# Kernel optimization log

Measured on AMD Instinct MI355X. Metric: run time of the kernel, lower is better.

The kernel has to match this reference:

```python
import jax, jax.numpy as jnp
import numpy as np
from jax import lax

D_MODEL = 1024
KERNEL = 7
EPS = 1e-8


def setup_inputs() -> dict:
    key = jax.random.key(0)
    ks = jax.random.split(key, 8)
    B, T, D = 4, 4096, D_MODEL
    x = jax.random.normal(ks[0], (B, T, D), dtype=jnp.float32)
    # rotary tables [T, D/2]
    pos = jnp.arange(T, dtype=jnp.float32)[:, None]
    inv_freq = 1.0 / (10000.0 ** (jnp.arange(D // 2, dtype=jnp.float32) / (D // 2)))
    ang = pos * inv_freq[None, :]
    sin = jnp.sin(ang)
    cos = jnp.cos(ang)
    # params
    W_proj = jax.random.normal(ks[1], (D, 2 * D), dtype=jnp.float32) * (1.0 / np.sqrt(D))
    b_proj = jnp.zeros((2 * D,), dtype=jnp.float32)
    dw_kernel = jax.random.normal(ks[2], (KERNEL, 1, D), dtype=jnp.float32) * 0.1  # [K,1,C] WIO depthwise
    dw_bias = jnp.zeros((D,), dtype=jnp.float32)
    gamma = jnp.ones((D,), dtype=jnp.float32)
    return {"x": x, "sin": sin, "cos": cos, "W_proj": W_proj, "b_proj": b_proj,
            "dw_kernel": dw_kernel, "dw_bias": dw_bias, "gamma": gamma}


def reference(x, sin, cos, W_proj, b_proj, dw_kernel, dw_bias, gamma):
    D = D_MODEL
    proj = jnp.einsum('btd,df->btf', x, W_proj) + b_proj          # [B,T,2D]
    x_a, x_b = proj[..., :D], proj[..., D:]
    # interleaved rotary: even/odd pairs
    x1 = x_a[..., 0::2]                                            # [B,T,D/2]
    x2 = x_a[..., 1::2]
    c = cos[None, :, :]
    s = sin[None, :, :]
    r1 = x1 * c - x2 * s
    r2 = x1 * s + x2 * c
    x_rot = jnp.stack([r1, r2], axis=-1).reshape(x_a.shape)        # re-interleave
    # depthwise conv1d, SAME padding
    conv = lax.conv_general_dilated(
        x_rot, dw_kernel, window_strides=(1,), padding='SAME',
        dimension_numbers=('NWC', 'WIO', 'NWC'), feature_group_count=D) + dw_bias
    act = conv * jax.nn.sigmoid(conv)                              # swish
    gated = act * jax.nn.sigmoid(x_b)
    rms = jnp.sqrt(jnp.mean(jnp.square(gated), axis=-1, keepdims=True) + EPS)
    return gamma * (gated / rms)
```

## Files before the change

### kernel.cpp

```cpp
#include <hip/hip_runtime.h>
#include <stdint.h>

#define D_MODEL 1024
#define T_LEN   4096
#define B_SZ    4
#define NROWS   (B_SZ * T_LEN)
#define NPROJ   (2 * D_MODEL)
#define CHUNK   16

#define BM 256
#define BN 256
#define BK 64
#define NT (D_MODEL / BK)

typedef __attribute__((ext_vector_type(8))) __bf16 bf16x8;
typedef __attribute__((ext_vector_type(4))) float  f32x4;

using as1_void = __attribute__((address_space(1))) void;
using as3_void = __attribute__((address_space(3))) void;

__device__ inline float bf2f(unsigned short u) {
    union { unsigned int i; float f; } v; v.i = ((unsigned int)u) << 16; return v.f;
}
__device__ inline unsigned short f2bf(float f) {
    union { float f; unsigned int i; } v; v.f = f;
    return (unsigned short)((v.i + 0x7fffu + ((v.i >> 16) & 1u)) >> 16);
}
__device__ inline float sigmoidf(float x) { return 1.0f / (1.0f + __expf(-x)); }

__global__ __launch_bounds__(256) void k_cvt_x(const float* __restrict__ x,
                                               unsigned short* __restrict__ xb) {
    int i = (blockIdx.x * 256 + threadIdx.x) * 4;
    float4 v = *reinterpret_cast<const float4*>(x + i);
    ushort4 o;
    o.x = f2bf(v.x); o.y = f2bf(v.y); o.z = f2bf(v.z); o.w = f2bf(v.w);
    *reinterpret_cast<ushort4*>(xb + i) = o;
}

__global__ __launch_bounds__(256) void k_cvt_w(const float* __restrict__ W,
                                               unsigned short* __restrict__ wt) {
    __shared__ unsigned short tile[32][33];
    int n0 = blockIdx.x * 32, k0 = blockIdx.y * 32;
    int c = threadIdx.x & 31, r = threadIdx.x >> 5;
    #pragma unroll
    for (int i = 0; i < 4; i++) {
        int kk = r + i * 8;
        tile[kk][c] = f2bf(W[(uint64_t)(k0 + kk) * NPROJ + n0 + c]);
    }
    __syncthreads();
    #pragma unroll
    for (int i = 0; i < 4; i++) {
        int nn = r + i * 8;
        wt[(uint64_t)(n0 + nn) * D_MODEL + k0 + c] = tile[c][nn];
    }
}

__global__ __launch_bounds__(512, 2) void k_gemm(const unsigned short* __restrict__ xb,
                                                 const unsigned short* __restrict__ wt,
                                                 const float* __restrict__ bias,
                                                 unsigned short* __restrict__ projb) {
    __shared__ __align__(16) unsigned short As[2 * BM * BK];
    __shared__ __align__(16) unsigned short Bs[2 * BM * BK];

    const int tid  = threadIdx.x;
    const int lane = tid & 63;
    const int w    = tid >> 6;
    const int wm   = w >> 2;
    const int wn   = w & 3;

    const int bid = blockIdx.x;
    const int wg  = (bid & 7) * 64 + (bid >> 3);
    const int n0  = (wg >> 6) * BN;
    const int m0  = (wg & 63) * BM;

    const int srow = tid >> 3;
    const int scol = ((tid & 7) ^ (srow & 7)) * 8;
    const int fr   = lane & 15;
    const int fq   = lane >> 4;

    f32x4 acc[8][4] = {};

    auto STAGE = [&](int buf, int ks) {
        #pragma unroll
        for (int i = 0; i < 4; ++i) {
            const unsigned short* ga = xb + (uint64_t)(m0 + i * 64 + srow) * D_MODEL + ks + scol;
            __builtin_amdgcn_global_load_lds((as1_void*)(void*)ga,
                (as3_void*)(void*)&As[buf * (BM * BK) + i * 4096 + w * 512], 16, 0, 0);
        }
        #pragma unroll
        for (int i = 0; i < 4; ++i) {
            const unsigned short* gb = wt + (uint64_t)(n0 + i * 64 + srow) * D_MODEL + ks + scol;
            __builtin_amdgcn_global_load_lds((as1_void*)(void*)gb,
                (as3_void*)(void*)&Bs[buf * (BM * BK) + i * 4096 + w * 512], 16, 0, 0);
        }
    };

    STAGE(0, 0);
    __syncthreads();

    for (int t = 0; t < NT; ++t) {
        const int cur = t & 1;
        if (t + 1 < NT) STAGE(1 - cur, (t + 1) * BK);

        const unsigned short* Ab = &As[cur * (BM * BK)];
        const unsigned short* Bb = &Bs[cur * (BM * BK)];
        #pragma unroll
        for (int kk = 0; kk < BK; kk += 32) {
            const int slot = (kk >> 3) + fq;
            bf16x8 b[4];
            #pragma unroll
            for (int n = 0; n < 4; n++) {
                const int rb = wn * 64 + n * 16 + fr;
                b[n] = *reinterpret_cast<const bf16x8*>(&Bb[rb * 64 + ((slot ^ (fr & 7)) * 8)]);
            }
            #pragma unroll
            for (int m = 0; m < 8; m++) {
                const int ra = wm * 128 + m * 16 + fr;
                bf16x8 a = *reinterpret_cast<const bf16x8*>(&Ab[ra * 64 + ((slot ^ (fr & 7)) * 8)]);
                #pragma unroll
                for (int n = 0; n < 4; n++)
                    acc[m][n] = __builtin_amdgcn_mfma_f32_16x16x32_bf16(a, b[n], acc[m][n], 0, 0, 0);
            }
        }
        __syncthreads();
    }

    #pragma unroll
    for (int m = 0; m < 8; m++) {
        const int grow = m0 + wm * 128 + m * 16 + fq * 4;
        #pragma unroll
        for (int n = 0; n < 4; n++) {
            const int gcol = n0 + wn * 64 + n * 16 + fr;
            const float bv = bias[gcol];
            #pragma unroll
            for (int r = 0; r < 4; r++) {
                projb[(uint64_t)(grow + r) * NPROJ + gcol] = f2bf(acc[m][n][r] + bv);
            }
        }
    }
}

__global__ __launch_bounds__(512) void k_post(const unsigned short* __restrict__ projb,
                                              const float* __restrict__ sinp,
                                              const float* __restrict__ cosp,
                                              const float* __restrict__ kw,
                                              const float* __restrict__ dwb,
                                              const float* __restrict__ gamma,
                                              float* __restrict__ out) {
    const int blk  = blockIdx.x;
    const int b    = blk / (T_LEN / CHUNK);
    const int t0   = (blk % (T_LEN / CHUNK)) * CHUNK;
    const int c    = threadIdx.x;
    const int d0   = c * 2;
    const uint64_t bbase = (uint64_t)b * T_LEN;

    float kwv[7][2];
    #pragma unroll
    for (int j = 0; j < 7; j++) {
        kwv[j][0] = kw[j * D_MODEL + d0];
        kwv[j][1] = kw[j * D_MODEL + d0 + 1];
    }
    const float bv0 = dwb[d0], bv1 = dwb[d0 + 1];
    const float gm0 = gamma[d0], gm1 = gamma[d0 + 1];

    __shared__ float red[2][8];

    auto load_rope = [&](int tj, float& o0, float& o1) {
        if ((unsigned)tj < (unsigned)T_LEN) {
            ushort2 u = *reinterpret_cast<const ushort2*>(projb + (bbase + tj) * NPROJ + d0);
            float cv = cosp[(uint64_t)tj * (D_MODEL / 2) + c];
            float sv = sinp[(uint64_t)tj * (D_MODEL / 2) + c];
            float x0 = bf2f(u.x), x1 = bf2f(u.y);
            o0 = x0 * cv - x1 * sv;
            o1 = x0 * sv + x1 * cv;
        } else { o0 = 0.f; o1 = 0.f; }
    };

    float rg[6][2];
    #pragma unroll
    for (int j = 0; j < 6; j++) load_rope(t0 - 3 + j, rg[j][0], rg[j][1]);
    float nx0, nx1;
    load_rope(t0 + 3, nx0, nx1);

    ushort2 xb_cur = *reinterpret_cast<const ushort2*>(projb + (bbase + t0) * NPROJ + D_MODEL + d0);

    for (int t = t0; t < t0 + CHUNK; ++t) {
        const float r60 = nx0, r61 = nx1;

        float acc0 = rg[0][0] * kwv[0][0] + rg[1][0] * kwv[1][0] + rg[2][0] * kwv[2][0]
                   + rg[3][0] * kwv[3][0] + rg[4][0] * kwv[4][0] + rg[5][0] * kwv[5][0]
                   + r60 * kwv[6][0] + bv0;
        float acc1 = rg[0][1] * kwv[0][1] + rg[1][1] * kwv[1][1] + rg[2][1] * kwv[2][1]
                   + rg[3][1] * kwv[3][1] + rg[4][1] * kwv[4][1] + rg[5][1] * kwv[5][1]
                   + r61 * kwv[6][1] + bv1;

        load_rope(t + 4, nx0, nx1);
        const ushort2 xb_use = xb_cur;
        if (t + 1 < t0 + CHUNK) {
            xb_cur = *reinterpret_cast<const ushort2*>(projb + (bbase + t + 1) * NPROJ + D_MODEL + d0);
        }

        float a0 = acc0 * sigmoidf(acc0);
        float a1 = acc1 * sigmoidf(acc1);
        float g0 = a0 * sigmoidf(bf2f(xb_use.x));
        float g1 = a1 * sigmoidf(bf2f(xb_use.y));

        float ssq = g0 * g0 + g1 * g1;
        #pragma unroll
        for (int off = 32; off; off >>= 1) ssq += __shfl_down(ssq, off);
        const int p = t & 1;
        if ((threadIdx.x & 63) == 0) red[p][threadIdx.x >> 6] = ssq;
        __syncthreads();
        float total = red[p][0] + red[p][1] + red[p][2] + red[p][3]
                    + red[p][4] + red[p][5] + red[p][6] + red[p][7];
        const float inv = 1.0f / sqrtf(total * (1.0f / (float)D_MODEL) + 1e-8f);

        float2 o;
        o.x = g0 * inv * gm0;
        o.y = g1 * inv * gm1;
        *reinterpret_cast<float2*>(out + (bbase + t) * D_MODEL + d0) = o;

        #pragma unroll
        for (int j = 0; j < 5; j++) { rg[j][0] = rg[j + 1][0]; rg[j][1] = rg[j + 1][1]; }
        rg[5][0] = r60; rg[5][1] = r61;
    }
}

extern "C" void kernel_launch(void* const* d_in, const int* in_sizes, int n_in,
                              void* d_out, int out_size, void* d_ws, size_t ws_size,
                              hipStream_t stream) {
    const float* x     = (const float*)d_in[0];
    const float* sinp  = (const float*)d_in[1];
    const float* cosp  = (const float*)d_in[2];
    const float* W     = (const float*)d_in[3];
    const float* bproj = (const float*)d_in[4];
    const float* dwk   = (const float*)d_in[5];
    const float* dwb   = (const float*)d_in[6];
    const float* gamma = (const float*)d_in[7];
    float* out = (float*)d_out;

    unsigned short* xb    = (unsigned short*)d_ws;
    unsigned short* wt    = xb + (size_t)NROWS * D_MODEL;
    unsigned short* projb = wt + (size_t)NPROJ * D_MODEL;

    k_cvt_x<<<(NROWS * D_MODEL) / (256 * 4), 256, 0, stream>>>(x, xb);
    k_cvt_w<<<dim3(NPROJ / 32, D_MODEL / 32), 256, 0, stream>>>(W, wt);
    k_gemm<<<(NPROJ / BN) * (NROWS / BM), 512, 0, stream>>>(xb, wt, bproj, projb);
    k_post<<<B_SZ * (T_LEN / CHUNK), 512, 0, stream>>>(projb, sinp, cosp, dwk, dwb, gamma, out);
}
```

Baseline: 149.0 us.

## Deepen GEMM pipeline to 4-stage LDS ring with BK=32 and manual vmcnt waits

```diff
diff --git a/kernel.cpp b/kernel.cpp
--- a/kernel.cpp
+++ b/kernel.cpp
@@ -10,8 +10,9 @@
 
 #define BM 256
 #define BN 256
-#define BK 64
-#define NT (D_MODEL / BK)
+#define BK2 32
+#define NT2 (D_MODEL / BK2)
+#define NBUF 4
 
 typedef __attribute__((ext_vector_type(8))) __bf16 bf16x8;
 typedef __attribute__((ext_vector_type(4))) float  f32x4;
@@ -59,8 +60,8 @@
                                                  const unsigned short* __restrict__ wt,
                                                  const float* __restrict__ bias,
                                                  unsigned short* __restrict__ projb) {
-    __shared__ __align__(16) unsigned short As[2 * BM * BK];
-    __shared__ __align__(16) unsigned short Bs[2 * BM * BK];
+    __shared__ __align__(16) unsigned short As[NBUF * BM * BK2];
+    __shared__ __align__(16) unsigned short Bs[NBUF * BM * BK2];
 
     const int tid  = threadIdx.x;
     const int lane = tid & 63;
@@ -73,56 +74,65 @@
     const int n0  = (wg >> 6) * BN;
     const int m0  = (wg & 63) * BM;
 
-    const int srow = tid >> 3;
-    const int scol = ((tid & 7) ^ (srow & 7)) * 8;
+    const int srow = tid >> 2;
+    const int skey = (tid >> 3) & 3;
+    const int scol = ((tid & 3) ^ skey) * 8;
     const int fr   = lane & 15;
     const int fq   = lane >> 4;
 
     f32x4 acc[8][4] = {};
 
-    auto STAGE = [&](int buf, int ks) {
-        #pragma unroll
-        for (int i = 0; i < 4; ++i) {
-            const unsigned short* ga = xb + (uint64_t)(m0 + i * 64 + srow) * D_MODEL + ks + scol;
+    auto STAGE = [&](int tk) {
+        const int buf = tk & 3;
+        const int ks  = tk * BK2;
+        #pragma unroll
+        for (int i = 0; i < 2; ++i) {
+            const unsigned short* ga = xb + (uint64_t)(m0 + i * 128 + srow) * D_MODEL + ks + scol;
             __builtin_amdgcn_global_load_lds((as1_void*)(void*)ga,
-                (as3_void*)(void*)&As[buf * (BM * BK) + i * 4096 + w * 512], 16, 0, 0);
-        }
-        #pragma unroll
-        for (int i = 0; i < 4; ++i) {
-            const unsigned short* gb = wt + (uint64_t)(n0 + i * 64 + srow) * D_MODEL + ks + scol;
+                (as3_void*)(void*)&As[buf * 8192 + i * 4096 + w * 512], 16, 0, 0);
+        }
+        #pragma unroll
+        for (int i = 0; i < 2; ++i) {
+            const unsigned short* gb = wt + (uint64_t)(n0 + i * 128 + srow) * D_MODEL + ks + scol;
             __builtin_amdgcn_global_load_lds((as1_void*)(void*)gb,
-                (as3_void*)(void*)&Bs[buf * (BM * BK) + i * 4096 + w * 512], 16, 0, 0);
+                (as3_void*)(void*)&Bs[buf * 8192 + i * 4096 + w * 512], 16, 0, 0);
         }
     };
 
-    STAGE(0, 0);
-    __syncthreads();
-
-    for (int t = 0; t < NT; ++t) {
-        const int cur = t & 1;
-        if (t + 1 < NT) STAGE(1 - cur, (t + 1) * BK);
-
-        const unsigned short* Ab = &As[cur * (BM * BK)];
-        const unsigned short* Bb = &Bs[cur * (BM * BK)];
-        #pragma unroll
-        for (int kk = 0; kk < BK; kk += 32) {
-            const int slot = (kk >> 3) + fq;
-            bf16x8 b[4];
+    STAGE(0); STAGE(1); STAGE(2);
+    asm volatile("s_waitcnt vmcnt(8)" ::: "memory");
+    __builtin_amdgcn_s_barrier();
+    __builtin_amdgcn_sched_barrier(0);
+
+    for (int t = 0; t < NT2; ++t) {
+        if (t + 3 < NT2) STAGE(t + 3);
+
+        const unsigned short* Ab = &As[(t & 3) * 8192];
+        const unsigned short* Bb = &Bs[(t & 3) * 8192];
+        bf16x8 a[8], b[4];
+        #pragma unroll
+        for (int n = 0; n < 4; n++) {
+            const int rb = wn * 64 + n * 16 + fr;
+            b[n] = *reinterpret_cast<const bf16x8*>(&Bb[rb * 32 + ((fq ^ ((rb >> 1) & 3)) * 8)]);
+        }
+        #pragma unroll
+        for (int m = 0; m < 8; m++) {
+            const int ra = wm * 128 + m * 16 + fr;
+            a[m] = *reinterpret_cast<const bf16x8*>(&Ab[ra * 32 + ((fq ^ ((ra >> 1) & 3)) * 8)]);
+        }
+        #pragma unroll
+        for (int m = 0; m < 8; m++)
             #pragma unroll
-            for (int n = 0; n < 4; n++) {
-                const int rb = wn * 64 + n * 16 + fr;
-                b[n] = *reinterpret_cast<const bf16x8*>(&Bb[rb * 64 + ((slot ^ (fr & 7)) * 8)]);
-            }
-            #pragma unroll
-            for (int m = 0; m < 8; m++) {
-                const int ra = wm * 128 + m * 16 + fr;
-                bf16x8 a = *reinterpret_cast<const bf16x8*>(&Ab[ra * 64 + ((slot ^ (fr & 7)) * 8)]);
-                #pragma unroll
-                for (int n = 0; n < 4; n++)
-                    acc[m][n] = __builtin_amdgcn_mfma_f32_16x16x32_bf16(a, b[n], acc[m][n], 0, 0, 0);
-            }
-        }
-        __syncthreads();
+            for (int n = 0; n < 4; n++)
+                acc[m][n] = __builtin_amdgcn_mfma_f32_16x16x32_bf16(a[m], b[n], acc[m][n], 0, 0, 0);
+
+        if (t < NT2 - 1) {
+            if (t + 3 < NT2)      asm volatile("s_waitcnt vmcnt(8)" ::: "memory");
+            else if (t + 2 < NT2) asm volatile("s_waitcnt vmcnt(4)" ::: "memory");
+            else                  asm volatile("s_waitcnt vmcnt(0)" ::: "memory");
+            __builtin_amdgcn_s_barrier();
+            __builtin_amdgcn_sched_barrier(0);
+        }
     }
 
     #pragma unroll
```

Result: slower. 162.2 us (+8.9%).

## Fuse rotary and gate sigmoid into GEMM epilogue, merge convert kernels

Applied to the files above, without the earlier changes.

```diff
diff --git a/kernel.cpp b/kernel.cpp
--- a/kernel.cpp
+++ b/kernel.cpp
@@ -28,36 +28,41 @@
 }
 __device__ inline float sigmoidf(float x) { return 1.0f / (1.0f + __expf(-x)); }
 
-__global__ __launch_bounds__(256) void k_cvt_x(const float* __restrict__ x,
-                                               unsigned short* __restrict__ xb) {
-    int i = (blockIdx.x * 256 + threadIdx.x) * 4;
-    float4 v = *reinterpret_cast<const float4*>(x + i);
-    ushort4 o;
-    o.x = f2bf(v.x); o.y = f2bf(v.y); o.z = f2bf(v.z); o.w = f2bf(v.w);
-    *reinterpret_cast<ushort4*>(xb + i) = o;
-}
-
-__global__ __launch_bounds__(256) void k_cvt_w(const float* __restrict__ W,
-                                               unsigned short* __restrict__ wt) {
+__global__ __launch_bounds__(256) void k_cvt(const float* __restrict__ x,
+                                             unsigned short* __restrict__ xb,
+                                             const float* __restrict__ W,
+                                             unsigned short* __restrict__ wt) {
     __shared__ unsigned short tile[32][33];
-    int n0 = blockIdx.x * 32, k0 = blockIdx.y * 32;
-    int c = threadIdx.x & 31, r = threadIdx.x >> 5;
-    #pragma unroll
-    for (int i = 0; i < 4; i++) {
-        int kk = r + i * 8;
-        tile[kk][c] = f2bf(W[(uint64_t)(k0 + kk) * NPROJ + n0 + c]);
-    }
-    __syncthreads();
-    #pragma unroll
-    for (int i = 0; i < 4; i++) {
-        int nn = r + i * 8;
-        wt[(uint64_t)(n0 + nn) * D_MODEL + k0 + c] = tile[c][nn];
+    int bid = blockIdx.x;
+    if (bid < (NROWS * D_MODEL) / (256 * 4)) {
+        int i = (bid * 256 + threadIdx.x) * 4;
+        float4 v = *reinterpret_cast<const float4*>(x + i);
+        ushort4 o;
+        o.x = f2bf(v.x); o.y = f2bf(v.y); o.z = f2bf(v.z); o.w = f2bf(v.w);
+        *reinterpret_cast<ushort4*>(xb + i) = o;
+    } else {
+        bid -= (NROWS * D_MODEL) / (256 * 4);
+        int n0 = (bid & 63) * 32, k0 = (bid >> 6) * 32;
+        int c = threadIdx.x & 31, r = threadIdx.x >> 5;
+        #pragma unroll
+        for (int i = 0; i < 4; i++) {
+            int kk = r + i * 8;
+            tile[kk][c] = f2bf(W[(uint64_t)(k0 + kk) * NPROJ + n0 + c]);
+        }
+        __syncthreads();
+        #pragma unroll
+        for (int i = 0; i < 4; i++) {
+            int nn = r + i * 8;
+            wt[(uint64_t)(n0 + nn) * D_MODEL + k0 + c] = tile[c][nn];
+        }
     }
 }
 
 __global__ __launch_bounds__(512, 2) void k_gemm(const unsigned short* __restrict__ xb,
                                                  const unsigned short* __restrict__ wt,
                                                  const float* __restrict__ bias,
+                                                 const float* __restrict__ sinp,
+                                                 const float* __restrict__ cosp,
                                                  unsigned short* __restrict__ projb) {
     __shared__ __align__(16) unsigned short As[2 * BM * BK];
     __shared__ __align__(16) unsigned short Bs[2 * BM * BK];
@@ -125,24 +130,46 @@
         __syncthreads();
     }
 
-    #pragma unroll
-    for (int m = 0; m < 8; m++) {
-        const int grow = m0 + wm * 128 + m * 16 + fq * 4;
-        #pragma unroll
-        for (int n = 0; n < 4; n++) {
-            const int gcol = n0 + wn * 64 + n * 16 + fr;
-            const float bv = bias[gcol];
-            #pragma unroll
-            for (int r = 0; r < 4; r++) {
-                projb[(uint64_t)(grow + r) * NPROJ + gcol] = f2bf(acc[m][n][r] + bv);
+    if (n0 < D_MODEL) {
+        #pragma unroll
+        for (int m = 0; m < 8; m++) {
+            const int grow = m0 + wm * 128 + m * 16 + fq * 4;
+            #pragma unroll
+            for (int n = 0; n < 4; n++) {
+                const int gcol = n0 + wn * 64 + n * 16 + fr;
+                const float bv = bias[gcol];
+                const int pidx = gcol >> 1;
+                const bool evn = (gcol & 1) == 0;
+                #pragma unroll
+                for (int r = 0; r < 4; r++) {
+                    const int trow = (grow + r) & (T_LEN - 1);
+                    float v = acc[m][n][r] + bv;
+                    float other = __shfl_xor(v, 1);
+                    float cv = cosp[(uint64_t)trow * (D_MODEL / 2) + pidx];
+                    float sv = sinp[(uint64_t)trow * (D_MODEL / 2) + pidx];
+                    float ro = evn ? (v * cv - other * sv) : (other * sv + v * cv);
+                    projb[(uint64_t)(grow + r) * NPROJ + gcol] = f2bf(ro);
+                }
+            }
+        }
+    } else {
+        #pragma unroll
+        for (int m = 0; m < 8; m++) {
+            const int grow = m0 + wm * 128 + m * 16 + fq * 4;
+            #pragma unroll
+            for (int n = 0; n < 4; n++) {
+                const int gcol = n0 + wn * 64 + n * 16 + fr;
+                const float bv = bias[gcol];
+                #pragma unroll
+                for (int r = 0; r < 4; r++) {
+                    projb[(uint64_t)(grow + r) * NPROJ + gcol] = f2bf(sigmoidf(acc[m][n][r] + bv));
+                }
             }
         }
     }
 }
 
 __global__ __launch_bounds__(512) void k_post(const unsigned short* __restrict__ projb,
-                                              const float* __restrict__ sinp,
-                                              const float* __restrict__ cosp,
                                               const float* __restrict__ kw,
                                               const float* __restrict__ dwb,
                                               const float* __restrict__ gamma,
@@ -165,22 +192,18 @@
 
     __shared__ float red[2][8];
 
-    auto load_rope = [&](int tj, float& o0, float& o1) {
+    auto load_row = [&](int tj, float& o0, float& o1) {
         if ((unsigned)tj < (unsigned)T_LEN) {
             ushort2 u = *reinterpret_cast<const ushort2*>(projb + (bbase + tj) * NPROJ + d0);
-            float cv = cosp[(uint64_t)tj * (D_MODEL / 2) + c];
-            float sv = sinp[(uint64_t)tj * (D_MODEL / 2) + c];
-            float x0 = bf2f(u.x), x1 = bf2f(u.y);
-            o0 = x0 * cv - x1 * sv;
-            o1 = x0 * sv + x1 * cv;
+            o0 = bf2f(u.x); o1 = bf2f(u.y);
         } else { o0 = 0.f; o1 = 0.f; }
     };
 
     float rg[6][2];
     #pragma unroll
-    for (int j = 0; j < 6; j++) load_rope(t0 - 3 + j, rg[j][0], rg[j][1]);
+    for (int j = 0; j < 6; j++) load_row(t0 - 3 + j, rg[j][0], rg[j][1]);
     float nx0, nx1;
-    load_rope(t0 + 3, nx0, nx1);
+    load_row(t0 + 3, nx0, nx1);
 
     ushort2 xb_cur = *reinterpret_cast<const ushort2*>(projb + (bbase + t0) * NPROJ + D_MODEL + d0);
 
@@ -194,7 +217,7 @@
                    + rg[3][1] * kwv[3][1] + rg[4][1] * kwv[4][1] + rg[5][1] * kwv[5][1]
                    + r61 * kwv[6][1] + bv1;
 
-        load_rope(t + 4, nx0, nx1);
+        load_row(t + 4, nx0, nx1);
         const ushort2 xb_use = xb_cur;
         if (t + 1 < t0 + CHUNK) {
             xb_cur = *reinterpret_cast<const ushort2*>(projb + (bbase + t + 1) * NPROJ + D_MODEL + d0);
@@ -202,8 +225,8 @@
 
         float a0 = acc0 * sigmoidf(acc0);
         float a1 = acc1 * sigmoidf(acc1);
-        float g0 = a0 * sigmoidf(bf2f(xb_use.x));
-        float g1 = a1 * sigmoidf(bf2f(xb_use.y));
+        float g0 = a0 * bf2f(xb_use.x);
+        float g1 = a1 * bf2f(xb_use.y);
 
         float ssq = g0 * g0 + g1 * g1;
         #pragma unroll
@@ -243,8 +266,9 @@
     unsigned short* wt    = xb + (size_t)NROWS * D_MODEL;
     unsigned short* projb = wt + (size_t)NPROJ * D_MODEL;
 
-    k_cvt_x<<<(NROWS * D_MODEL) / (256 * 4), 256, 0, stream>>>(x, xb);
-    k_cvt_w<<<dim3(NPROJ / 32, D_MODEL / 32), 256, 0, stream>>>(W, wt);
-    k_gemm<<<(NPROJ / BN) * (NROWS / BM), 512, 0, stream>>>(xb, wt, bproj, projb);
-    k_post<<<B_SZ * (T_LEN / CHUNK), 512, 0, stream>>>(projb, sinp, cosp, dwk, dwb, gamma, out);
-}
+    const int cvt_x_blocks = (NROWS * D_MODEL) / (256 * 4);
+    const int cvt_w_blocks = (NPROJ / 32) * (D_MODEL / 32);
+    k_cvt<<<cvt_x_blocks + cvt_w_blocks, 256, 0, stream>>>(x, xb, W, wt);
+    k_gemm<<<(NPROJ / BN) * (NROWS / BM), 512, 0, stream>>>(xb, wt, bproj, sinp, cosp, projb);
+    k_post<<<B_SZ * (T_LEN / CHUNK), 512, 0, stream>>>(projb, dwk, dwb, gamma, out);
+}
```

Measured after the change: 152.1 us. +2.1%, slower.
